# Performance work log

Measured on AMD Instinct MI355X. Metric: run time of the kernel, lower is better.

Reference implementation:

```python
import jax, jax.numpy as jnp
import numpy as np

H, W = 101, 31
HEADS, DH, FREQ = 8, 64, 64
C_DIM = 256
INNER = HEADS * DH
EPS = 1e-5


def _conv2d(x, w, b):
    # x: (B, Cin, H, W), w: (Cout, Cin, 3, 3) -> SAME padding, stride 1
    y = jax.lax.conv_general_dilated(x, w, (1, 1), 'SAME',
                                     dimension_numbers=('NCHW', 'OIHW', 'NCHW'))
    return y + b[None, :, None, None]


def setup_inputs() -> dict:
    key = jax.random.key(0)
    ks = jax.random.split(key, 8)
    B = 32
    N = H * W  # 3131
    s = 0.02
    x = jax.random.normal(ks[0], (B, N, C_DIM), jnp.float32)
    conv_fx_w = jax.random.normal(ks[1], (INNER, C_DIM, 3, 3), jnp.float32) * s
    conv_fx_b = jnp.zeros((INNER,), jnp.float32)
    conv_x_w = jax.random.normal(ks[2], (INNER, C_DIM, 3, 3), jnp.float32) * s
    conv_x_b = jnp.zeros((INNER,), jnp.float32)
    gate_w = jax.random.normal(ks[3], (FREQ, DH), jnp.float32) * s  # nn.Linear weight (out,in)
    gate_b = jnp.zeros((FREQ,), jnp.float32)
    temperature = jnp.full((1, HEADS, 1, 1), 0.5, jnp.float32)
    ln_gamma = jnp.ones((FREQ, DH), jnp.float32)
    ln_beta = jnp.zeros((FREQ, DH), jnp.float32)
    mlp_w = jax.random.normal(ks[4], (DH, DH), jnp.float32) * s
    out_w = jax.random.normal(ks[5], (C_DIM, INNER), jnp.float32) * s
    out_b = jnp.zeros((C_DIM,), jnp.float32)
    # fixed (non-trainable) spectral basis, L2-normalized per row like F.normalize(dim=-1)
    inver = jax.random.normal(ks[6], (N, FREQ), jnp.float32)
    inver = inver / jnp.linalg.norm(inver, axis=-1, keepdims=True)
    return dict(x=x, conv_fx_w=conv_fx_w, conv_fx_b=conv_fx_b, conv_x_w=conv_x_w,
                conv_x_b=conv_x_b, gate_w=gate_w, gate_b=gate_b,
                temperature=temperature, ln_gamma=ln_gamma, ln_beta=ln_beta,
                mlp_w=mlp_w, out_w=out_w, out_b=out_b, inver=inver)


def reference(x, conv_fx_w, conv_fx_b, conv_x_w, conv_x_b, gate_w, gate_b,
              temperature, ln_gamma, ln_beta, mlp_w, out_w, out_b, inver):
    B, N, C = x.shape
    xi = x.reshape(B, H, W, C).transpose(0, 3, 1, 2)  # (B, C, H, W)

    def proj(w, b):
        y = _conv2d(xi, w, b)                                  # (B, inner, H, W)
        return y.transpose(0, 2, 3, 1).reshape(B, N, HEADS, DH).transpose(0, 2, 1, 3)  # (B,h,N,d)

    fx_mid = proj(conv_fx_w, conv_fx_b)
    x_mid = proj(conv_x_w, conv_x_b)

    temp = jnp.clip(temperature, 0.1, 5.0)                      # (1,h,1,1)
    logits = jnp.einsum('bhnc,gc->bhng', x_mid, gate_w) + gate_b
    gate = jax.nn.softmax(logits / temp, axis=-1)               # (B,h,N,g)
    eigens = gate * inver[None, None]                           # (B,h,N,g)

    spec = jnp.einsum('bhnc,bhng->bhgc', fx_mid, eigens)        # (B,h,g,c)
    # LayerNorm over the trailing (g, c) axes jointly
    mu = spec.mean(axis=(-2, -1), keepdims=True)
    var = spec.var(axis=(-2, -1), keepdims=True)
    spec = (spec - mu) * jax.lax.rsqrt(var + EPS) * ln_gamma + ln_beta

    out_spec = jnp.einsum('bhgi,io->bhgo', spec, mlp_w)
    out_x = jnp.einsum('bhgc,bhng->bhnc', out_spec, eigens)     # (B,h,N,c)
    out_x = out_x.transpose(0, 2, 1, 3).reshape(B, N, HEADS * DH)
    return jnp.einsum('bnd,cd->bnc', out_x, out_w) + out_b      # to_out (dropout is identity)
```

## Files before the change

### kernel.cpp

```cpp
#include <hip/hip_runtime.h>
#include <hip/hip_bf16.h>
#include <stdint.h>

#define HH 101
#define WW 31
#define NN 3131
#define NPAD 3136
#define BB 32
#define NH 8
#define CDIM 256
#define GG 64
#define HP 103
#define WP 33

typedef __attribute__((ext_vector_type(8))) short bf16x8;
typedef __attribute__((ext_vector_type(4))) float f32x4;
typedef __attribute__((ext_vector_type(4))) unsigned short ushort4_t;
typedef __attribute__((ext_vector_type(8))) unsigned short ushort8_t;
typedef __attribute__((ext_vector_type(4))) float float4_t;

static __device__ __forceinline__ unsigned short f2bf(float f) {
  union { float f; uint32_t u; } v; v.f = f;
  uint32_t u = v.u;
  return (unsigned short)((u + 0x7fffu + ((u >> 16) & 1u)) >> 16);
}
static __device__ __forceinline__ float bf2f(unsigned short h) {
  union { uint32_t u; float f; } v; v.u = ((uint32_t)h) << 16;
  return v.f;
}
static __device__ __forceinline__ void gload_lds16(const void* g, void* l) {
  __builtin_amdgcn_global_load_lds((const __attribute__((address_space(1))) void*)g,
                                   (__attribute__((address_space(3))) void*)l, 16, 0, 0);
}
static __device__ __forceinline__ int xcd_swz(int bid, int nwg) {
  int q = nwg >> 3, r = nwg & 7;
  int xcd = bid & 7, pos = bid >> 3;
  int base = (xcd < r) ? xcd * (q + 1) : r * (q + 1) + (xcd - r) * q;
  return base + pos;
}

__global__ void k_pad(const float* __restrict__ x, unsigned short* __restrict__ xpad, int b0) {
  const int xx = blockIdx.x, yy = blockIdx.y, b = blockIdx.z;
  const int t = threadIdx.x;
  ushort4_t o; o.x = 0; o.y = 0; o.z = 0; o.w = 0;
  if (yy >= 1 && yy <= HH && xx >= 1 && xx <= WW) {
    const int n = (yy - 1) * WW + (xx - 1);
    const float4_t v = *(const float4_t*)(x + (((int64_t)(b0 + b) * NN + n) * CDIM + t * 4));
    o.x = f2bf(v.x); o.y = f2bf(v.y); o.z = f2bf(v.z); o.w = f2bf(v.w);
  }
  *(ushort4_t*)(xpad + (((int64_t)b * HP + yy) * WP + xx) * CDIM + t * 4) = o;
}

__global__ void k_wpack(const float* __restrict__ fxw, const float* __restrict__ xw,
                        const float* __restrict__ fxb, const float* __restrict__ xb,
                        const float* __restrict__ gw,
                        unsigned short* __restrict__ Wb, float* __restrict__ bias,
                        unsigned short* __restrict__ gwb) {
  int tid = blockIdx.x * blockDim.x + threadIdx.x;
  const int total = 9 * 1024 * 256;
  if (tid < total) {
    int cin = tid & 255; int rest = tid >> 8; int co = rest & 1023; int t = rest >> 10;
    float v = (co < 512) ? fxw[(int64_t)co * 2304 + cin * 9 + t]
                         : xw[(int64_t)(co - 512) * 2304 + cin * 9 + t];
    Wb[tid] = f2bf(v);
  }
  if (tid < 1024) bias[tid] = (tid < 512) ? fxb[tid] : xb[tid - 512];
  if (tid < 4096) gwb[tid] = f2bf(gw[tid]);
}

__global__ void k_pprep(const float* __restrict__ mlp, const float* __restrict__ outw,
                        unsigned short* __restrict__ Pt) {
  int h = blockIdx.x >> 6, i = blockIdx.x & 63, co = threadIdx.x;
  float a = 0.f;
  for (int c = 0; c < 64; ++c) a += mlp[i * 64 + c] * outw[(int64_t)co * 512 + h * 64 + c];
  Pt[((int64_t)h * 256 + co) * 64 + i] = f2bf(a);
}

__global__ void k_padzero(unsigned short* __restrict__ fxT, unsigned short* __restrict__ xmid,
                          int CB) {
  int tid = blockIdx.x * blockDim.x + threadIdx.x;
  if (tid >= CB * 2560) return;
  {
    int j = tid % 5; int rc = tid / 5;
    fxT[(int64_t)rc * NPAD + NN + j] = 0;
  }
  {
    int d = tid & 63; int rest = tid >> 6;
    int j = rest % 5; int bh = rest / 5;
    xmid[((int64_t)bh * NPAD + NN + j) * 64 + d] = 0;
  }
}

__launch_bounds__(512, 2)
__global__ void k_conv8(const unsigned short* __restrict__ xpad,
                        const unsigned short* __restrict__ Wb,
                        const float* __restrict__ bias,
                        unsigned short* __restrict__ fxT,
                        unsigned short* __restrict__ xmid) {
  extern __shared__ unsigned short lds[];
  const int swz = xcd_swz(blockIdx.x, gridDim.x);
  const int r   = swz % 52;
  const int b   = swz / 52;
  const int bx  = r & 3;
  const int mt  = r >> 2;
  const int tid = threadIdx.x, wid = tid >> 6, lane = tid & 63;
  const int wm = wid & 3, wn = wid >> 2;
  const int arow = lane & 15, col16 = lane >> 4;
  const int n00 = mt * 256, co00 = bx * 256;

  const int srow = wid * 16 + (lane >> 2);
  const int tc   = ((lane & 3) ^ ((lane >> 3) & 3)) * 8;
  int na0 = n00 + srow;        if (na0 >= NN) na0 = NN - 1;
  int na1 = n00 + srow + 128;  if (na1 >= NN) na1 = NN - 1;
  const int y0 = na0 / WW, x0v = na0 % WW;
  const int y1 = na1 / WW, x1v = na1 % WW;
  const unsigned short* aS0 = xpad + ((int64_t)(b * HP + y0) * WP + x0v) * CDIM + tc;
  const unsigned short* aS1 = xpad + ((int64_t)(b * HP + y1) * WP + x1v) * CDIM + tc;
  const unsigned short* bS0 = Wb + (int64_t)(co00 + srow) * CDIM + tc;
  const unsigned short* bS1 = Wb + (int64_t)(co00 + srow + 128) * CDIM + tc;

  const int rdsz = (col16 ^ ((arow >> 1) & 3)) * 8;

  f32x4 acc[4][8] = {};
  bf16x8 a0[4], a1[4], b03[4], b47[4];

#define STAGE_A(s, kk, aoffv)                                        \
  { unsigned short* d = lds + (s) * 32768 + (kk) * 8192 + wid * 512; \
    gload_lds16(aS0 + (aoffv) + (kk) * 32, d);                       \
    gload_lds16(aS1 + (aoffv) + (kk) * 32, d + 4096); }
#define STAGE_B(s, kk, boffv)                                                \
  { unsigned short* d = lds + (s) * 32768 + 16384 + (kk) * 8192 + wid * 512; \
    gload_lds16(bS0 + (boffv) + (kk) * 32, d);                               \
    gload_lds16(bS1 + (boffv) + (kk) * 32, d + 4096); }
#define KOFF(ks, aoffv, boffv)                              \
  { const int tap = (ks) >> 2;                              \
    const int dy = (tap >= 6) + (tap >= 3);                 \
    const int dx = tap - dy * 3;                            \
    const int cb = ((ks) & 3) << 6;                         \
    aoffv = (dy * WP + dx) * CDIM + cb;                     \
    boffv = tap * 262144 + cb; }
#define RD_A(dst, s, kk, mf)                                                             \
  dst = *(const bf16x8*)(lds + (s) * 32768 + (kk) * 8192 +                               \
                         (wm * 64 + (mf) * 16 + arow) * 32 + rdsz);
#define RD_B(dst, s, kk, nf)                                                             \
  dst = *(const bf16x8*)(lds + (s) * 32768 + 16384 + (kk) * 8192 +                       \
                         (wn * 128 + (nf) * 16 + arow) * 32 + rdsz);
#define MFMA16(aset, bset, nbase)                                                        \
  __builtin_amdgcn_s_setprio(1);                                                         \
  _Pragma("unroll")                                                                      \
  for (int mf = 0; mf < 4; ++mf) {                                                       \
    _Pragma("unroll")                                                                    \
    for (int nf = 0; nf < 4; ++nf)                                                       \
      acc[mf][(nbase) + nf] =                                                            \
        __builtin_amdgcn_mfma_f32_16x16x32_bf16(aset[mf], bset[nf], acc[mf][(nbase) + nf], 0, 0, 0); \
  }                                                                                      \
  __builtin_amdgcn_s_setprio(0);

  int aoff0, boff0;
  KOFF(0, aoff0, boff0);
  STAGE_A(0, 0, aoff0); STAGE_B(0, 0, boff0);
  STAGE_A(0, 1, aoff0); STAGE_B(0, 1, boff0);
  asm volatile("s_waitcnt vmcnt(4)" ::: "memory");
  __builtin_amdgcn_s_barrier();
  asm volatile("" ::: "memory");
  #pragma unroll
  for (int i = 0; i < 4; ++i) { RD_A(a0[i], 0, 0, i); }
  #pragma unroll
  for (int i = 0; i < 4; ++i) { RD_B(b03[i], 0, 0, i); }

  #pragma unroll 1
  for (int t = 0; t < 36; ++t) {
    const int cur = t & 1, nxt = cur ^ 1;
    const int tn = (t < 35) ? t + 1 : 35;
    int aoffn, boffn;
    KOFF(tn, aoffn, boffn);

    #pragma unroll
    for (int i = 0; i < 4; ++i) { RD_B(b47[i], cur, 0, 4 + i); }
    STAGE_A(nxt, 0, aoffn);
    asm volatile("s_waitcnt lgkmcnt(4)" ::: "memory");
    __builtin_amdgcn_sched_barrier(0);
    MFMA16(a0, b03, 0);

    STAGE_B(nxt, 0, boffn);
    asm volatile("s_waitcnt vmcnt(4)" ::: "memory");
    __builtin_amdgcn_s_barrier();
    asm volatile("" ::: "memory");
    #pragma unroll
    for (int i = 0; i < 4; ++i) { RD_A(a1[i], cur, 1, i); }
    #pragma unroll
    for (int i = 0; i < 4; ++i) { RD_B(b03[i], cur, 1, i); }
    asm volatile("s_waitcnt lgkmcnt(8)" ::: "memory");
    __builtin_amdgcn_sched_barrier(0);
    MFMA16(a0, b47, 4);

    #pragma unroll
    for (int i = 0; i < 4; ++i) { RD_B(b47[i], cur, 1, 4 + i); }
    STAGE_A(nxt, 1, aoffn);
    asm volatile("s_waitcnt lgkmcnt(4)" ::: "memory");
    __builtin_amdgcn_sched_barrier(0);
    MFMA16(a1, b03, 0);

    STAGE_B(nxt, 1, boffn);
    asm volatile("s_waitcnt vmcnt(4)" ::: "memory");
    __builtin_amdgcn_s_barrier();
    asm volatile("" ::: "memory");
    #pragma unroll
    for (int i = 0; i < 4; ++i) { RD_A(a0[i], nxt, 0, i); }
    #pragma unroll
    for (int i = 0; i < 4; ++i) { RD_B(b03[i], nxt, 0, i); }
    asm volatile("s_waitcnt lgkmcnt(8)" ::: "memory");
    __builtin_amdgcn_sched_barrier(0);
    MFMA16(a1, b47, 4);
  }

  asm volatile("s_waitcnt vmcnt(0) lgkmcnt(0)" ::: "memory");

  const int rowoff = col16 * 4;
  #pragma unroll
  for (int mf = 0; mf < 4; ++mf) {
    const int nr = n00 + wm * 64 + mf * 16 + rowoff;
    #pragma unroll
    for (int nf = 0; nf < 8; ++nf) {
      const int co = co00 + wn * 128 + nf * 16 + arow;
      const float bvs = bias[co];
      const float v0 = acc[mf][nf][0] + bvs;
      const float v1 = acc[mf][nf][1] + bvs;
      const float v2 = acc[mf][nf][2] + bvs;
      const float v3 = acc[mf][nf][3] + bvs;
      if (bx < 2) {
        const int h = co >> 6, c = co & 63;
        unsigned short* dst = fxT + ((int64_t)((b * NH + h) * 64 + c)) * NPAD + nr;
        if (nr + 3 < NN) {
          ushort4_t o; o.x = f2bf(v0); o.y = f2bf(v1); o.z = f2bf(v2); o.w = f2bf(v3);
          *(ushort4_t*)dst = o;
        } else {
          if (nr + 0 < NN) dst[0] = f2bf(v0);
          if (nr + 1 < NN) dst[1] = f2bf(v1);
          if (nr + 2 < NN) dst[2] = f2bf(v2);
          if (nr + 3 < NN) dst[3] = f2bf(v3);
        }
      } else {
        const int h = (co >> 6) & 7, d = co & 63;
        unsigned short* dst = xmid + ((int64_t)(b * NH + h) * NPAD + nr) * 64 + d;
        if (nr + 0 < NN) dst[0] = f2bf(v0);
        if (nr + 1 < NN) dst[64] = f2bf(v1);
        if (nr + 2 < NN) dst[128] = f2bf(v2);
        if (nr + 3 < NN) dst[192] = f2bf(v3);
      }
    }
  }
#undef STAGE_A
#undef STAGE_B
#undef KOFF
#undef RD_A
#undef RD_B
#undef MFMA16
}

__global__ void k_eig(const unsigned short* __restrict__ xmid,
                      const unsigned short* __restrict__ gwb,
                      const float* __restrict__ gateb,
                      const float* __restrict__ temperature,
                      const float* __restrict__ inver,
                      unsigned short* __restrict__ eigT,
                      unsigned short* __restrict__ eigN) {
  __shared__ unsigned short egN[64 * 72];
  __shared__ unsigned short egT[64 * 72];
  const int nt = blockIdx.x, h = blockIdx.y, b = blockIdx.z;
  const int tid = threadIdx.x;
  const int w = tid >> 6, lane = tid & 63;
  const int n0 = nt * 64 + w * 16;
  const int bh = b * NH + h;
  float tv = temperature[h];
  tv = fminf(fmaxf(tv, 0.1f), 5.0f);
  const float itemp = 1.0f / tv;
  const int arow = lane & 15;
  const int koff = (lane >> 4) * 8;
  const unsigned short* aptr = xmid + ((int64_t)bh * NPAD + (n0 + arow)) * 64 + koff;
  bf16x8 a0 = *(const bf16x8*)(aptr);
  bf16x8 a1 = *(const bf16x8*)(aptr + 32);
  f32x4 acc[4] = {};
  #pragma unroll
  for (int ng = 0; ng < 4; ++ng) {
    const unsigned short* bptr = gwb + (ng * 16 + arow) * 64 + koff;
    bf16x8 b0 = *(const bf16x8*)(bptr);
    bf16x8 b1 = *(const bf16x8*)(bptr + 32);
    acc[ng] = __builtin_amdgcn_mfma_f32_16x16x32_bf16(a0, b0, acc[ng], 0, 0, 0);
    acc[ng] = __builtin_amdgcn_mfma_f32_16x16x32_bf16(a1, b1, acc[ng], 0, 0, 0);
  }
  #pragma unroll
  for (int r = 0; r < 4; ++r) {
    const int nl = w * 16 + ((lane >> 4) << 2) + r;
    const int n = nt * 64 + nl;
    float vals[4];
    #pragma unroll
    for (int ng = 0; ng < 4; ++ng) vals[ng] = (acc[ng][r] + gateb[ng * 16 + arow]) * itemp;
    float mx = fmaxf(fmaxf(vals[0], vals[1]), fmaxf(vals[2], vals[3]));
    #pragma unroll
    for (int s = 1; s < 16; s <<= 1) mx = fmaxf(mx, __shfl_xor(mx, s));
    float ex[4]; float sum = 0.f;
    #pragma unroll
    for (int ng = 0; ng < 4; ++ng) { ex[ng] = __expf(vals[ng] - mx); sum += ex[ng]; }
    #pragma unroll
    for (int s = 1; s < 16; s <<= 1) sum += __shfl_xor(sum, s);
    const float inv = 1.0f / sum;
    const bool valid = (n < NN);
    #pragma unroll
    for (int ng = 0; ng < 4; ++ng) {
      const int g = ng * 16 + arow;
      float iv = valid ? inver[(int64_t)n * GG + g] : 0.f;
      unsigned short u = valid ? f2bf(ex[ng] * inv * iv) : (unsigned short)0;
      egN[nl * 72 + g] = u;
      egT[g * 72 + nl] = u;
    }
  }
  __syncthreads();
  const int row = tid >> 2, c0 = (tid & 3) << 4;
  {
    ushort8_t v0 = *(ushort8_t*)&egN[row * 72 + c0];
    ushort8_t v1 = *(ushort8_t*)&egN[row * 72 + c0 + 8];
    unsigned short* dst = eigN + ((int64_t)bh * NPAD + nt * 64 + row) * 64 + c0;
    *(ushort8_t*)dst = v0; *(ushort8_t*)(dst + 8) = v1;
  }
  {
    ushort8_t v0 = *(ushort8_t*)&egT[row * 72 + c0];
    ushort8_t v1 = *(ushort8_t*)&egT[row * 72 + c0 + 8];
    unsigned short* dst = eigT + ((int64_t)(bh * 64 + row)) * NPAD + nt * 64 + c0;
    *(ushort8_t*)dst = v0; *(ushort8_t*)(dst + 8) = v1;
  }
}

__launch_bounds__(256, 1)
__global__ void k_specln(const unsigned short* __restrict__ eigT,
                         const unsigned short* __restrict__ fxT,
                         const float* __restrict__ gamma, const float* __restrict__ beta,
                         const unsigned short* __restrict__ Pt,
                         unsigned short* __restrict__ m2t) {
  extern __shared__ char sm[];
  float* sacc = (float*)sm;
  unsigned short* specb = (unsigned short*)(sm + 66560);
  float* red = (float*)(sm + 74752);
  unsigned short* mstrip = (unsigned short*)(sm + 74784);
  const int bhl = blockIdx.x;
  const int h = bhl & 7, bl = bhl >> 3;
  const int tid = threadIdx.x, w = tid >> 6, lane = tid & 63;
  const int arow = lane & 15, col16 = lane >> 4;
  const int koff = col16 * 8;
  const unsigned short* eb = eigT + (int64_t)bhl * 64 * NPAD;
  const unsigned short* fb = fxT + (int64_t)bhl * 64 * NPAD;

  const int ks0 = (98 * w) >> 2, ks1 = (98 * (w + 1)) >> 2;
  f32x4 acc[4][4] = {};
  for (int ks = ks0; ks < ks1; ++ks) {
    const int k0 = ks * 32 + koff;
    bf16x8 av[4], bv[4];
    #pragma unroll
    for (int mg = 0; mg < 4; ++mg) av[mg] = *(const bf16x8*)(eb + (int64_t)(mg * 16 + arow) * NPAD + k0);
    #pragma unroll
    for (int ng = 0; ng < 4; ++ng) bv[ng] = *(const bf16x8*)(fb + (int64_t)(ng * 16 + arow) * NPAD + k0);
    #pragma unroll
    for (int mg = 0; mg < 4; ++mg)
      #pragma unroll
      for (int ng = 0; ng < 4; ++ng)
        acc[mg][ng] = __builtin_amdgcn_mfma_f32_16x16x32_bf16(av[mg], bv[ng], acc[mg][ng], 0, 0, 0);
  }
  float* pw = sacc + w * (64 * 65);
  #pragma unroll
  for (int mg = 0; mg < 4; ++mg)
    #pragma unroll
    for (int ng = 0; ng < 4; ++ng)
      #pragma unroll
      for (int r = 0; r < 4; ++r)
        pw[(mg * 16 + col16 * 4 + r) * 65 + ng * 16 + arow] = acc[mg][ng][r];
  __syncthreads();

  float vloc[16];
  float lsum = 0.f, lsq = 0.f;
  #pragma unroll
  for (int idx = 0; idx < 16; ++idx) {
    const int e = tid + idx * 256;
    const int g = e >> 6, c = e & 63;
    float v = sacc[g * 65 + c] + sacc[4160 + g * 65 + c] +
              sacc[8320 + g * 65 + c] + sacc[12480 + g * 65 + c];
    vloc[idx] = v; lsum += v; lsq += v * v;
  }
  #pragma unroll
  for (int s = 1; s < 64; s <<= 1) { lsum += __shfl_xor(lsum, s); lsq += __shfl_xor(lsq, s); }
  if (lane == 0) { red[w] = lsum; red[4 + w] = lsq; }
  __syncthreads();
  const float tsum = red[0] + red[1] + red[2] + red[3];
  const float tsq = red[4] + red[5] + red[6] + red[7];
  const float mu = tsum * (1.0f / 4096.0f);
  const float var = tsq * (1.0f / 4096.0f) - mu * mu;
  const float rs = rsqrtf(var + 1e-5f);
  #pragma unroll
  for (int idx = 0; idx < 16; ++idx) {
    const int e = tid + idx * 256;
    const int g = e >> 6, c = e & 63;
    float sv = (vloc[idx] - mu) * rs * gamma[e] + beta[e];
    specb[g * 64 + ((((c >> 3) ^ (g & 7))) << 3) + (c & 7)] = f2bf(sv);
  }
  __syncthreads();

  f32x4 a2[4][4] = {};
  const unsigned short* pth = Pt + ((int64_t)h * 256 + w * 64) * 64;
  #pragma unroll
  for (int kk = 0; kk < 2; ++kk) {
    const int i0 = kk * 32 + koff;
    const int i8 = (i0 >> 3);
    bf16x8 av2[4], bv2[4];
    #pragma unroll
    for (int mg = 0; mg < 4; ++mg) {
      const int g = mg * 16 + arow;
      av2[mg] = *(const bf16x8*)(specb + g * 64 + ((i8 ^ (g & 7)) << 3));
    }
    #pragma unroll
    for (int ng = 0; ng < 4; ++ng)
      bv2[ng] = *(const bf16x8*)(pth + (ng * 16 + arow) * 64 + i0);
    #pragma unroll
    for (int mg = 0; mg < 4; ++mg)
      #pragma unroll
      for (int ng = 0; ng < 4; ++ng)
        a2[mg][ng] = __builtin_amdgcn_mfma_f32_16x16x32_bf16(av2[mg], bv2[ng], a2[mg][ng], 0, 0, 0);
  }
  unsigned short* ms = mstrip + w * (64 * 72);
  #pragma unroll
  for (int mg = 0; mg < 4; ++mg)
    #pragma unroll
    for (int ng = 0; ng < 4; ++ng)
      #pragma unroll
      for (int r = 0; r < 4; ++r)
        ms[(ng * 16 + arow) * 72 + mg * 16 + col16 * 4 + r] = f2bf(a2[mg][ng][r]);
  __syncthreads();
  #pragma unroll
  for (int e0 = 0; e0 < 8; ++e0) {
    const int e = lane + e0 * 64;
    const int row = e >> 3, g8 = e & 7;
    ushort8_t v = *(ushort8_t*)&ms[row * 72 + g8 * 8];
    *(ushort8_t*)(m2t + ((int64_t)(bl * 256 + w * 64 + row)) * 512 + h * 64 + g8 * 8) = v;
  }
}

__launch_bounds__(256)
__global__ void k_out(const unsigned short* __restrict__ eigN,
                      const unsigned short* __restrict__ m2t,
                      const float* __restrict__ outb,
                      float* __restrict__ out, int b0) {
  const int swz = xcd_swz(blockIdx.x, gridDim.x);
  const int ct = swz & 1;
  const int mt = (swz >> 1) % 25;
  const int b  = swz / 50;
  const int w = threadIdx.x >> 6, lane = threadIdx.x & 63;
  const int wm = w >> 1, wn = w & 1;
  const int arow = lane & 15, koff = (lane >> 4) * 8;
  const int co0 = ct * 128 + wn * 64;
  const int n0 = mt * 128 + wm * 64;
  f32x4 acc[4][4] = {};
  const unsigned short* ebase = eigN + (int64_t)b * NH * NPAD * 64;
  const unsigned short* mbase = m2t + (int64_t)b * 256 * 512;
  for (int ks = 0; ks < 16; ++ks) {
    const int hh = ks >> 1;
    const int g0 = (ks & 1) * 32 + koff;
    bf16x8 av[4], bv[4];
    #pragma unroll
    for (int mg = 0; mg < 4; ++mg) {
      int n = n0 + mg * 16 + arow;
      if (n > NPAD - 1) n = NPAD - 1;
      av[mg] = *(const bf16x8*)(ebase + ((int64_t)hh * NPAD + n) * 64 + g0);
    }
    #pragma unroll
    for (int ng = 0; ng < 4; ++ng)
      bv[ng] = *(const bf16x8*)(mbase + (int64_t)(co0 + ng * 16 + arow) * 512 + ks * 32 + koff);
    #pragma unroll
    for (int mg = 0; mg < 4; ++mg)
      #pragma unroll
      for (int ng = 0; ng < 4; ++ng)
        acc[mg][ng] = __builtin_amdgcn_mfma_f32_16x16x32_bf16(av[mg], bv[ng], acc[mg][ng], 0, 0, 0);
  }
  #pragma unroll
  for (int mg = 0; mg < 4; ++mg) {
    const int nr = n0 + mg * 16 + ((lane >> 4) << 2);
    #pragma unroll
    for (int ng = 0; ng < 4; ++ng) {
      const int co = co0 + ng * 16 + arow;
      const float bv = outb[co];
      #pragma unroll
      for (int r = 0; r < 4; ++r) {
        if (nr + r < NN)
          out[((int64_t)(b0 + b) * NN + nr + r) * 256 + co] = acc[mg][ng][r] + bv;
      }
    }
  }
}

extern "C" void kernel_launch(void* const* d_in, const int* in_sizes, int n_in,
                              void* d_out, int out_size, void* d_ws, size_t ws_size,
                              hipStream_t stream) {
  const float* x     = (const float*)d_in[0];
  const float* fxw   = (const float*)d_in[1];
  const float* fxb   = (const float*)d_in[2];
  const float* xw    = (const float*)d_in[3];
  const float* xb    = (const float*)d_in[4];
  const float* gw    = (const float*)d_in[5];
  const float* gb    = (const float*)d_in[6];
  const float* temp  = (const float*)d_in[7];
  const float* gamma = (const float*)d_in[8];
  const float* beta  = (const float*)d_in[9];
  const float* mlp   = (const float*)d_in[10];
  const float* outw  = (const float*)d_in[11];
  const float* outb  = (const float*)d_in[12];
  const float* inver = (const float*)d_in[13];
  float* out = (float*)d_out;
  char* ws = (char*)d_ws;
  (void)in_sizes; (void)n_in; (void)out_size;

  hipFuncSetAttribute(reinterpret_cast<const void*>(k_conv8),
                      hipFuncAttributeMaxDynamicSharedMemorySize, 131072);
  hipFuncSetAttribute(reinterpret_cast<const void*>(k_specln),
                      hipFuncAttributeMaxDynamicSharedMemorySize, 131072);

  int CB = 1;
  {
    const int cands[6] = {32, 16, 8, 4, 2, 1};
    for (int i = 0; i < 6; ++i) {
      unsigned long long need = 4993024ull + (unsigned long long)cands[i] * 14847488ull;
      if (need <= (unsigned long long)ws_size) { CB = cands[i]; break; }
    }
  }

  unsigned short* Wb   = (unsigned short*)(ws + 0);
  float*          bias = (float*)(ws + 4718592);
  unsigned short* gwb  = (unsigned short*)(ws + 4722688);
  unsigned short* Pt   = (unsigned short*)(ws + 4730880);
  const size_t F0      = 4993024;
  const size_t szXpad  = (size_t)CB * 1740288;
  const size_t szM2t   = (size_t)CB * 262144;
  const size_t szBig   = (size_t)CB * 3211264;
  unsigned short* xpad = (unsigned short*)(ws + F0);
  unsigned short* m2t  = (unsigned short*)(ws + F0 + szXpad);
  unsigned short* fxT  = (unsigned short*)(ws + F0 + szXpad + szM2t);
  unsigned short* xmid = (unsigned short*)(ws + F0 + szXpad + szM2t + szBig);
  unsigned short* eigT = (unsigned short*)(ws + F0 + szXpad + szM2t + 2 * szBig);
  unsigned short* eigN = (unsigned short*)(ws + F0 + szXpad + szM2t + 3 * szBig);

  k_wpack<<<dim3(9216), dim3(256), 0, stream>>>(fxw, xw, fxb, xb, gw, Wb, bias, gwb);
  k_pprep<<<dim3(512), dim3(256), 0, stream>>>(mlp, outw, Pt);

  for (int b0 = 0; b0 < BB; b0 += CB) {
    k_pad<<<dim3(WP, HP, CB), dim3(64), 0, stream>>>(x, xpad, b0);
    k_padzero<<<dim3(CB * 10), dim3(256), 0, stream>>>(fxT, xmid, CB);
    k_conv8<<<dim3(52 * CB), dim3(512), 131072, stream>>>(xpad, Wb, bias, fxT, xmid);
    k_eig<<<dim3(49, 8, CB), dim3(256), 0, stream>>>(xmid, gwb, gb, temp, inver, eigT, eigN);
    k_specln<<<dim3(CB * 8), dim3(256), 111648, stream>>>(eigT, fxT, gamma, beta, Pt, m2t);
    k_out<<<dim3(50 * CB), dim3(256), 0, stream>>>(eigN, m2t, outb, out, b0);
  }
}
```

Baseline: 884.9 us.

## Enlarge per-wave conv tile to 128x128 using four waves per block

The implicit-GEMM convolution kernel moves from 8 waves (512 threads) to 4 waves (256 threads) per 256x256 block tile. Each wave now computes a 128x128 sub-tile with 64 accumulators instead of 32, and loads four rows per staging step. The aim is to cut LDS reads per MFMA and raise arithmetic intensity per wave. In exchange, accumulator registers per thread double and fewer waves are available per CU to hide latency, with launch bounds set to one block.

```diff
diff --git a/kernel.cpp b/kernel.cpp
--- a/kernel.cpp
+++ b/kernel.cpp
@@ -91,7 +91,7 @@
   }
 }
 
-__launch_bounds__(512, 2)
+__launch_bounds__(256, 1)
 __global__ void k_conv8(const unsigned short* __restrict__ xpad,
                         const unsigned short* __restrict__ Wb,
                         const float* __restrict__ bias,
@@ -104,34 +104,39 @@
   const int bx  = r & 3;
   const int mt  = r >> 2;
   const int tid = threadIdx.x, wid = tid >> 6, lane = tid & 63;
-  const int wm = wid & 3, wn = wid >> 2;
+  const int wm = wid >> 1, wn = wid & 1;
   const int arow = lane & 15, col16 = lane >> 4;
   const int n00 = mt * 256, co00 = bx * 256;
 
-  const int srow = wid * 16 + (lane >> 2);
-  const int tc   = ((lane & 3) ^ ((lane >> 3) & 3)) * 8;
-  int na0 = n00 + srow;        if (na0 >= NN) na0 = NN - 1;
-  int na1 = n00 + srow + 128;  if (na1 >= NN) na1 = NN - 1;
-  const int y0 = na0 / WW, x0v = na0 % WW;
-  const int y1 = na1 / WW, x1v = na1 % WW;
-  const unsigned short* aS0 = xpad + ((int64_t)(b * HP + y0) * WP + x0v) * CDIM + tc;
-  const unsigned short* aS1 = xpad + ((int64_t)(b * HP + y1) * WP + x1v) * CDIM + tc;
-  const unsigned short* bS0 = Wb + (int64_t)(co00 + srow) * CDIM + tc;
-  const unsigned short* bS1 = Wb + (int64_t)(co00 + srow + 128) * CDIM + tc;
+  const int tc = ((lane & 3) ^ ((lane >> 3) & 3)) * 8;
+  const unsigned short* aS[4];
+  const unsigned short* bS[4];
+  #pragma unroll
+  for (int i = 0; i < 4; ++i) {
+    const int srow = wid * 64 + i * 16 + (lane >> 2);
+    int na = n00 + srow; if (na >= NN) na = NN - 1;
+    const int y = na / WW, xv = na % WW;
+    aS[i] = xpad + ((int64_t)(b * HP + y) * WP + xv) * CDIM + tc;
+    bS[i] = Wb + (int64_t)(co00 + srow) * CDIM + tc;
+  }
 
   const int rdsz = (col16 ^ ((arow >> 1) & 3)) * 8;
 
-  f32x4 acc[4][8] = {};
-  bf16x8 a0[4], a1[4], b03[4], b47[4];
-
-#define STAGE_A(s, kk, aoffv)                                        \
-  { unsigned short* d = lds + (s) * 32768 + (kk) * 8192 + wid * 512; \
-    gload_lds16(aS0 + (aoffv) + (kk) * 32, d);                       \
-    gload_lds16(aS1 + (aoffv) + (kk) * 32, d + 4096); }
-#define STAGE_B(s, kk, boffv)                                                \
-  { unsigned short* d = lds + (s) * 32768 + 16384 + (kk) * 8192 + wid * 512; \
-    gload_lds16(bS0 + (boffv) + (kk) * 32, d);                               \
-    gload_lds16(bS1 + (boffv) + (kk) * 32, d + 4096); }
+  f32x4 acc[8][8] = {};
+  bf16x8 a0[8], a1[8], b03[4], b47[4];
+
+#define STAGE_A(s, kk, aoffv)                                          \
+  { unsigned short* d = lds + (s) * 32768 + (kk) * 8192 + wid * 2048;  \
+    gload_lds16(aS[0] + (aoffv) + (kk) * 32, d);                       \
+    gload_lds16(aS[1] + (aoffv) + (kk) * 32, d + 512);                 \
+    gload_lds16(aS[2] + (aoffv) + (kk) * 32, d + 1024);                \
+    gload_lds16(aS[3] + (aoffv) + (kk) * 32, d + 1536); }
+#define STAGE_B(s, kk, boffv)                                                  \
+  { unsigned short* d = lds + (s) * 32768 + 16384 + (kk) * 8192 + wid * 2048;  \
+    gload_lds16(bS[0] + (boffv) + (kk) * 32, d);                               \
+    gload_lds16(bS[1] + (boffv) + (kk) * 32, d + 512);                         \
+    gload_lds16(bS[2] + (boffv) + (kk) * 32, d + 1024);                        \
+    gload_lds16(bS[3] + (boffv) + (kk) * 32, d + 1536); }
 #define KOFF(ks, aoffv, boffv)                              \
   { const int tap = (ks) >> 2;                              \
     const int dy = (tap >= 6) + (tap >= 3);                 \
@@ -139,32 +144,32 @@
     const int cb = ((ks) & 3) << 6;                         \
     aoffv = (dy * WP + dx) * CDIM + cb;                     \
     boffv = tap * 262144 + cb; }
-#define RD_A(dst, s, kk, mf)                                                             \
-  dst = *(const bf16x8*)(lds + (s) * 32768 + (kk) * 8192 +                               \
-                         (wm * 64 + (mf) * 16 + arow) * 32 + rdsz);
-#define RD_B(dst, s, kk, nf)                                                             \
-  dst = *(const bf16x8*)(lds + (s) * 32768 + 16384 + (kk) * 8192 +                       \
+#define RD_A(dst, s, kk, mf)                                                       \
+  dst = *(const bf16x8*)(lds + (s) * 32768 + (kk) * 8192 +                         \
+                         (wm * 128 + (mf) * 16 + arow) * 32 + rdsz);
+#define RD_B(dst, s, kk, nf)                                                       \
+  dst = *(const bf16x8*)(lds + (s) * 32768 + 16384 + (kk) * 8192 +                 \
                          (wn * 128 + (nf) * 16 + arow) * 32 + rdsz);
-#define MFMA16(aset, bset, nbase)                                                        \
-  __builtin_amdgcn_s_setprio(1);                                                         \
-  _Pragma("unroll")                                                                      \
-  for (int mf = 0; mf < 4; ++mf) {                                                       \
-    _Pragma("unroll")                                                                    \
-    for (int nf = 0; nf < 4; ++nf)                                                       \
-      acc[mf][(nbase) + nf] =                                                            \
-        __builtin_amdgcn_mfma_f32_16x16x32_bf16(aset[mf], bset[nf], acc[mf][(nbase) + nf], 0, 0, 0); \
-  }                                                                                      \
+#define MFMA32(aset, bset, nbase)                                                  \
+  __builtin_amdgcn_s_setprio(1);                                                   \
+  _Pragma("unroll")                                                                \
+  for (int mf = 0; mf < 8; ++mf) {                                                 \
+    _Pragma("unroll")                                                              \
+    for (int j = 0; j < 4; ++j)                                                    \
+      acc[mf][(nbase) + j] =                                                       \
+        __builtin_amdgcn_mfma_f32_16x16x32_bf16(aset[mf], bset[j], acc[mf][(nbase) + j], 0, 0, 0); \
+  }                                                                                \
   __builtin_amdgcn_s_setprio(0);
 
   int aoff0, boff0;
   KOFF(0, aoff0, boff0);
   STAGE_A(0, 0, aoff0); STAGE_B(0, 0, boff0);
   STAGE_A(0, 1, aoff0); STAGE_B(0, 1, boff0);
-  asm volatile("s_waitcnt vmcnt(4)" ::: "memory");
+  asm volatile("s_waitcnt vmcnt(8)" ::: "memory");
   __builtin_amdgcn_s_barrier();
   asm volatile("" ::: "memory");
   #pragma unroll
-  for (int i = 0; i < 4; ++i) { RD_A(a0[i], 0, 0, i); }
+  for (int i = 0; i < 8; ++i) { RD_A(a0[i], 0, 0, i); }
   #pragma unroll
   for (int i = 0; i < 4; ++i) { RD_B(b03[i], 0, 0, i); }
 
@@ -180,46 +185,46 @@
     STAGE_A(nxt, 0, aoffn);
     asm volatile("s_waitcnt lgkmcnt(4)" ::: "memory");
     __builtin_amdgcn_sched_barrier(0);
-    MFMA16(a0, b03, 0);
+    MFMA32(a0, b03, 0);
 
     STAGE_B(nxt, 0, boffn);
-    asm volatile("s_waitcnt vmcnt(4)" ::: "memory");
+    asm volatile("s_waitcnt vmcnt(8)" ::: "memory");
     __builtin_amdgcn_s_barrier();
     asm volatile("" ::: "memory");
     #pragma unroll
-    for (int i = 0; i < 4; ++i) { RD_A(a1[i], cur, 1, i); }
+    for (int i = 0; i < 8; ++i) { RD_A(a1[i], cur, 1, i); }
     #pragma unroll
     for (int i = 0; i < 4; ++i) { RD_B(b03[i], cur, 1, i); }
-    asm volatile("s_waitcnt lgkmcnt(8)" ::: "memory");
+    asm volatile("s_waitcnt lgkmcnt(12)" ::: "memory");
     __builtin_amdgcn_sched_barrier(0);
-    MFMA16(a0, b47, 4);
+    MFMA32(a0, b47, 4);
 
     #pragma unroll
     for (int i = 0; i < 4; ++i) { RD_B(b47[i], cur, 1, 4 + i); }
     STAGE_A(nxt, 1, aoffn);
     asm volatile("s_waitcnt lgkmcnt(4)" ::: "memory");
     __builtin_amdgcn_sched_barrier(0);
-    MFMA16(a1, b03, 0);
+    MFMA32(a1, b03, 0);
 
     STAGE_B(nxt, 1, boffn);
-    asm volatile("s_waitcnt vmcnt(4)" ::: "memory");
+    asm volatile("s_waitcnt vmcnt(8)" ::: "memory");
     __builtin_amdgcn_s_barrier();
     asm volatile("" ::: "memory");
     #pragma unroll
-    for (int i = 0; i < 4; ++i) { RD_A(a0[i], nxt, 0, i); }
+    for (int i = 0; i < 8; ++i) { RD_A(a0[i], nxt, 0, i); }
     #pragma unroll
     for (int i = 0; i < 4; ++i) { RD_B(b03[i], nxt, 0, i); }
-    asm volatile("s_waitcnt lgkmcnt(8)" ::: "memory");
+    asm volatile("s_waitcnt lgkmcnt(12)" ::: "memory");
     __builtin_amdgcn_sched_barrier(0);
-    MFMA16(a1, b47, 4);
+    MFMA32(a1, b47, 4);
   }
 
   asm volatile("s_waitcnt vmcnt(0) lgkmcnt(0)" ::: "memory");
 
   const int rowoff = col16 * 4;
   #pragma unroll
-  for (int mf = 0; mf < 4; ++mf) {
-    const int nr = n00 + wm * 64 + mf * 16 + rowoff;
+  for (int mf = 0; mf < 8; ++mf) {
+    const int nr = n00 + wm * 128 + mf * 16 + rowoff;
     #pragma unroll
     for (int nf = 0; nf < 8; ++nf) {
       const int co = co00 + wn * 128 + nf * 16 + arow;
@@ -255,7 +260,7 @@
 #undef KOFF
 #undef RD_A
 #undef RD_B
-#undef MFMA16
+#undef MFMA32
 }
 
 __global__ void k_eig(const unsigned short* __restrict__ xmid,
@@ -550,7 +555,7 @@
   for (int b0 = 0; b0 < BB; b0 += CB) {
     k_pad<<<dim3(WP, HP, CB), dim3(64), 0, stream>>>(x, xpad, b0);
     k_padzero<<<dim3(CB * 10), dim3(256), 0, stream>>>(fxT, xmid, CB);
-    k_conv8<<<dim3(52 * CB), dim3(512), 131072, stream>>>(xpad, Wb, bias, fxT, xmid);
+    k_conv8<<<dim3(52 * CB), dim3(256), 131072, stream>>>(xpad, Wb, bias, fxT, xmid);
     k_eig<<<dim3(49, 8, CB), dim3(256), 0, stream>>>(xmid, gwb, gb, temp, inver, eigT, eigN);
     k_specln<<<dim3(CB * 8), dim3(256), 111648, stream>>>(eigT, fxT, gamma, beta, Pt, m2t);
     k_out<<<dim3(50 * CB), dim3(256), 0, stream>>>(eigN, m2t, outb, out, b0);
```

New measurement: 968.3 us. 1.09x slower.

## Load conv weight fragments directly from global into registers, stage only activations in LDS

Applied to the files above, without the earlier changes.

The conv GEMM kernel stops staging the weight (B) tiles through LDS and has each wave load its B fragments straight from global memory into registers. LDS now holds only the double-buffered activation tiles, which halves dynamic shared memory from 128 KB to 64 KB and removes the B-side LDS reads. The intent is to cut LDS traffic and footprint, possibly allowing more occupancy. The cost is global/L2 latency on the B loads, which each wave issues redundantly, plus larger register pressure from four B fragment sets and a simpler interleave that waits lgkmcnt(0).

```diff
diff --git a/kernel.cpp b/kernel.cpp
--- a/kernel.cpp
+++ b/kernel.cpp
@@ -116,22 +116,17 @@
   const int y1 = na1 / WW, x1v = na1 % WW;
   const unsigned short* aS0 = xpad + ((int64_t)(b * HP + y0) * WP + x0v) * CDIM + tc;
   const unsigned short* aS1 = xpad + ((int64_t)(b * HP + y1) * WP + x1v) * CDIM + tc;
-  const unsigned short* bS0 = Wb + (int64_t)(co00 + srow) * CDIM + tc;
-  const unsigned short* bS1 = Wb + (int64_t)(co00 + srow + 128) * CDIM + tc;
+  const unsigned short* baseB = Wb + (int64_t)(co00 + wn * 128 + arow) * 256 + col16 * 8;
 
   const int rdsz = (col16 ^ ((arow >> 1) & 3)) * 8;
 
   f32x4 acc[4][8] = {};
-  bf16x8 a0[4], a1[4], b03[4], b47[4];
+  bf16x8 a0[4], a1[4], bq0[4], bq1[4], bq2[4], bq3[4];
 
 #define STAGE_A(s, kk, aoffv)                                        \
-  { unsigned short* d = lds + (s) * 32768 + (kk) * 8192 + wid * 512; \
+  { unsigned short* d = lds + (s) * 16384 + (kk) * 8192 + wid * 512; \
     gload_lds16(aS0 + (aoffv) + (kk) * 32, d);                       \
     gload_lds16(aS1 + (aoffv) + (kk) * 32, d + 4096); }
-#define STAGE_B(s, kk, boffv)                                                \
-  { unsigned short* d = lds + (s) * 32768 + 16384 + (kk) * 8192 + wid * 512; \
-    gload_lds16(bS0 + (boffv) + (kk) * 32, d);                               \
-    gload_lds16(bS1 + (boffv) + (kk) * 32, d + 4096); }
 #define KOFF(ks, aoffv, boffv)                              \
   { const int tap = (ks) >> 2;                              \
     const int dy = (tap >= 6) + (tap >= 3);                 \
@@ -139,34 +134,34 @@
     const int cb = ((ks) & 3) << 6;                         \
     aoffv = (dy * WP + dx) * CDIM + cb;                     \
     boffv = tap * 262144 + cb; }
-#define RD_A(dst, s, kk, mf)                                                             \
-  dst = *(const bf16x8*)(lds + (s) * 32768 + (kk) * 8192 +                               \
-                         (wm * 64 + (mf) * 16 + arow) * 32 + rdsz);
-#define RD_B(dst, s, kk, nf)                                                             \
-  dst = *(const bf16x8*)(lds + (s) * 32768 + 16384 + (kk) * 8192 +                       \
-                         (wn * 128 + (nf) * 16 + arow) * 32 + rdsz);
-#define MFMA16(aset, bset, nbase)                                                        \
-  __builtin_amdgcn_s_setprio(1);                                                         \
-  _Pragma("unroll")                                                                      \
-  for (int mf = 0; mf < 4; ++mf) {                                                       \
-    _Pragma("unroll")                                                                    \
-    for (int nf = 0; nf < 4; ++nf)                                                       \
-      acc[mf][(nbase) + nf] =                                                            \
+#define LDB(dst, boffv, kk, nf4)                                                    \
+  { _Pragma("unroll")                                                               \
+    for (int j = 0; j < 4; ++j)                                                     \
+      dst[j] = *(const bf16x8*)(baseB + ((nf4) + j) * 4096 + (boffv) + (kk) * 32); }
+#define RD_A4(dst, s, kk)                                                           \
+  { _Pragma("unroll")                                                               \
+    for (int i = 0; i < 4; ++i)                                                     \
+      dst[i] = *(const bf16x8*)(lds + (s) * 16384 + (kk) * 8192 +                   \
+                                (wm * 64 + i * 16 + arow) * 32 + rdsz); }
+#define MFMA16(aset, bset, nbase)                                                   \
+  __builtin_amdgcn_s_setprio(1);                                                    \
+  _Pragma("unroll")                                                                 \
+  for (int mf = 0; mf < 4; ++mf) {                                                  \
+    _Pragma("unroll")                                                               \
+    for (int nf = 0; nf < 4; ++nf)                                                  \
+      acc[mf][(nbase) + nf] =                                                       \
         __builtin_amdgcn_mfma_f32_16x16x32_bf16(aset[mf], bset[nf], acc[mf][(nbase) + nf], 0, 0, 0); \
-  }                                                                                      \
+  }                                                                                 \
   __builtin_amdgcn_s_setprio(0);
 
-  int aoff0, boff0;
-  KOFF(0, aoff0, boff0);
-  STAGE_A(0, 0, aoff0); STAGE_B(0, 0, boff0);
-  STAGE_A(0, 1, aoff0); STAGE_B(0, 1, boff0);
+  int aoff0, boffc;
+  KOFF(0, aoff0, boffc);
+  STAGE_A(0, 0, aoff0);
+  STAGE_A(0, 1, aoff0);
+  LDB(bq0, boffc, 0, 0);
   asm volatile("s_waitcnt vmcnt(4)" ::: "memory");
   __builtin_amdgcn_s_barrier();
   asm volatile("" ::: "memory");
-  #pragma unroll
-  for (int i = 0; i < 4; ++i) { RD_A(a0[i], 0, 0, i); }
-  #pragma unroll
-  for (int i = 0; i < 4; ++i) { RD_B(b03[i], 0, 0, i); }
 
   #pragma unroll 1
   for (int t = 0; t < 36; ++t) {
@@ -175,43 +170,29 @@
     int aoffn, boffn;
     KOFF(tn, aoffn, boffn);
 
-    #pragma unroll
-    for (int i = 0; i < 4; ++i) { RD_B(b47[i], cur, 0, 4 + i); }
+    LDB(bq1, boffc, 0, 4);
     STAGE_A(nxt, 0, aoffn);
-    asm volatile("s_waitcnt lgkmcnt(4)" ::: "memory");
+    STAGE_A(nxt, 1, aoffn);
+    RD_A4(a0, cur, 0);
+    asm volatile("s_waitcnt lgkmcnt(0)" ::: "memory");
     __builtin_amdgcn_sched_barrier(0);
-    MFMA16(a0, b03, 0);
-
-    STAGE_B(nxt, 0, boffn);
+    MFMA16(a0, bq0, 0);
+
+    LDB(bq2, boffc, 1, 0);
+    RD_A4(a1, cur, 1);
+    MFMA16(a0, bq1, 4);
+
+    LDB(bq3, boffc, 1, 4);
+    asm volatile("s_waitcnt lgkmcnt(0)" ::: "memory");
+    __builtin_amdgcn_sched_barrier(0);
+    MFMA16(a1, bq2, 0);
+
+    LDB(bq0, boffn, 0, 0);
+    MFMA16(a1, bq3, 4);
     asm volatile("s_waitcnt vmcnt(4)" ::: "memory");
     __builtin_amdgcn_s_barrier();
     asm volatile("" ::: "memory");
-    #pragma unroll
-    for (int i = 0; i < 4; ++i) { RD_A(a1[i], cur, 1, i); }
-    #pragma unroll
-    for (int i = 0; i < 4; ++i) { RD_B(b03[i], cur, 1, i); }
-    asm volatile("s_waitcnt lgkmcnt(8)" ::: "memory");
-    __builtin_amdgcn_sched_barrier(0);
-    MFMA16(a0, b47, 4);
-
-    #pragma unroll
-    for (int i = 0; i < 4; ++i) { RD_B(b47[i], cur, 1, 4 + i); }
-    STAGE_A(nxt, 1, aoffn);
-    asm volatile("s_waitcnt lgkmcnt(4)" ::: "memory");
-    __builtin_amdgcn_sched_barrier(0);
-    MFMA16(a1, b03, 0);
-
-    STAGE_B(nxt, 1, boffn);
-    asm volatile("s_waitcnt vmcnt(4)" ::: "memory");
-    __builtin_amdgcn_s_barrier();
-    asm volatile("" ::: "memory");
-    #pragma unroll
-    for (int i = 0; i < 4; ++i) { RD_A(a0[i], nxt, 0, i); }
-    #pragma unroll
-    for (int i = 0; i < 4; ++i) { RD_B(b03[i], nxt, 0, i); }
-    asm volatile("s_waitcnt lgkmcnt(8)" ::: "memory");
-    __builtin_amdgcn_sched_barrier(0);
-    MFMA16(a1, b47, 4);
+    boffc = boffn;
   }
 
   asm volatile("s_waitcnt vmcnt(0) lgkmcnt(0)" ::: "memory");
@@ -251,10 +232,9 @@
     }
   }
 #undef STAGE_A
-#undef STAGE_B
 #undef KOFF
-#undef RD_A
-#undef RD_B
+#undef LDB
+#undef RD_A4
 #undef MFMA16
 }
 
@@ -516,7 +496,7 @@
   (void)in_sizes; (void)n_in; (void)out_size;
 
   hipFuncSetAttribute(reinterpret_cast<const void*>(k_conv8),
-                      hipFuncAttributeMaxDynamicSharedMemorySize, 131072);
+                      hipFuncAttributeMaxDynamicSharedMemorySize, 65536);
   hipFuncSetAttribute(reinterpret_cast<const void*>(k_specln),
                       hipFuncAttributeMaxDynamicSharedMemorySize, 131072);
 
@@ -550,7 +530,7 @@
   for (int b0 = 0; b0 < BB; b0 += CB) {
     k_pad<<<dim3(WP, HP, CB), dim3(64), 0, stream>>>(x, xpad, b0);
     k_padzero<<<dim3(CB * 10), dim3(256), 0, stream>>>(fxT, xmid, CB);
-    k_conv8<<<dim3(52 * CB), dim3(512), 131072, stream>>>(xpad, Wb, bias, fxT, xmid);
+    k_conv8<<<dim3(52 * CB), dim3(512), 65536, stream>>>(xpad, Wb, bias, fxT, xmid);
     k_eig<<<dim3(49, 8, CB), dim3(256), 0, stream>>>(xmid, gwb, gb, temp, inver, eigT, eigN);
     k_specln<<<dim3(CB * 8), dim3(256), 111648, stream>>>(eigT, fxT, gamma, beta, Pt, m2t);
     k_out<<<dim3(50 * CB), dim3(256), 0, stream>>>(eigN, m2t, outb, out, b0);
```

After: 1.509 ms. 70.5% more time.

## Fuse gate softmax and eigen computation into conv epilogue, dropping xmid buffer

Applied to the files above, without the earlier changes.

The x-projection half of the conv kernel no longer writes x_mid to global memory. It stages each head's tile in LDS, runs the gate matmul with MFMA, applies the temperature softmax times the basis, and writes eigT and eigN directly. This removes the separate k_eig launch and the round trip of the x_mid tensor through global memory, and it shrinks the workspace so larger batch chunks can fit. In exchange the x-projection blocks get a heavier epilogue with extra barriers and register pressure, which makes their work uneven against the fx blocks.

```diff
diff --git a/kernel.cpp b/kernel.cpp
--- a/kernel.cpp
+++ b/kernel.cpp
@@ -76,27 +76,24 @@
   Pt[((int64_t)h * 256 + co) * 64 + i] = f2bf(a);
 }
 
-__global__ void k_padzero(unsigned short* __restrict__ fxT, unsigned short* __restrict__ xmid,
-                          int CB) {
+__global__ void k_padzero(unsigned short* __restrict__ fxT, int CB) {
   int tid = blockIdx.x * blockDim.x + threadIdx.x;
   if (tid >= CB * 2560) return;
-  {
-    int j = tid % 5; int rc = tid / 5;
-    fxT[(int64_t)rc * NPAD + NN + j] = 0;
-  }
-  {
-    int d = tid & 63; int rest = tid >> 6;
-    int j = rest % 5; int bh = rest / 5;
-    xmid[((int64_t)bh * NPAD + NN + j) * 64 + d] = 0;
-  }
+  int j = tid % 5; int rc = tid / 5;
+  fxT[(int64_t)rc * NPAD + NN + j] = 0;
 }
 
 __launch_bounds__(512, 2)
 __global__ void k_conv8(const unsigned short* __restrict__ xpad,
                         const unsigned short* __restrict__ Wb,
                         const float* __restrict__ bias,
+                        const unsigned short* __restrict__ gwb,
+                        const float* __restrict__ gateb,
+                        const float* __restrict__ temperature,
+                        const float* __restrict__ inver,
                         unsigned short* __restrict__ fxT,
-                        unsigned short* __restrict__ xmid) {
+                        unsigned short* __restrict__ eigT,
+                        unsigned short* __restrict__ eigN) {
   extern __shared__ unsigned short lds[];
   const int swz = xcd_swz(blockIdx.x, gridDim.x);
   const int r   = swz % 52;
@@ -217,18 +214,19 @@
   asm volatile("s_waitcnt vmcnt(0) lgkmcnt(0)" ::: "memory");
 
   const int rowoff = col16 * 4;
-  #pragma unroll
-  for (int mf = 0; mf < 4; ++mf) {
-    const int nr = n00 + wm * 64 + mf * 16 + rowoff;
-    #pragma unroll
-    for (int nf = 0; nf < 8; ++nf) {
-      const int co = co00 + wn * 128 + nf * 16 + arow;
-      const float bvs = bias[co];
-      const float v0 = acc[mf][nf][0] + bvs;
-      const float v1 = acc[mf][nf][1] + bvs;
-      const float v2 = acc[mf][nf][2] + bvs;
-      const float v3 = acc[mf][nf][3] + bvs;
-      if (bx < 2) {
+
+  if (bx < 2) {
+    #pragma unroll
+    for (int mf = 0; mf < 4; ++mf) {
+      const int nr = n00 + wm * 64 + mf * 16 + rowoff;
+      #pragma unroll
+      for (int nf = 0; nf < 8; ++nf) {
+        const int co = co00 + wn * 128 + nf * 16 + arow;
+        const float bvs = bias[co];
+        const float v0 = acc[mf][nf][0] + bvs;
+        const float v1 = acc[mf][nf][1] + bvs;
+        const float v2 = acc[mf][nf][2] + bvs;
+        const float v3 = acc[mf][nf][3] + bvs;
         const int h = co >> 6, c = co & 63;
         unsigned short* dst = fxT + ((int64_t)((b * NH + h) * 64 + c)) * NPAD + nr;
         if (nr + 3 < NN) {
@@ -240,13 +238,103 @@
           if (nr + 2 < NN) dst[2] = f2bf(v2);
           if (nr + 3 < NN) dst[3] = f2bf(v3);
         }
-      } else {
-        const int h = (co >> 6) & 7, d = co & 63;
-        unsigned short* dst = xmid + ((int64_t)(b * NH + h) * NPAD + nr) * 64 + d;
-        if (nr + 0 < NN) dst[0] = f2bf(v0);
-        if (nr + 1 < NN) dst[64] = f2bf(v1);
-        if (nr + 2 < NN) dst[128] = f2bf(v2);
-        if (nr + 3 < NN) dst[192] = f2bf(v3);
+      }
+    }
+  } else {
+    const int hbase = (bx - 2) * 4;
+    unsigned short* xm = lds;
+    #pragma unroll 1
+    for (int hh = 0; hh < 2; ++hh) {
+      __syncthreads();
+      unsigned short* xmw = xm + wn * (256 * 72);
+      #pragma unroll
+      for (int mf = 0; mf < 4; ++mf) {
+        const int nr = wm * 64 + mf * 16 + rowoff;
+        #pragma unroll
+        for (int j = 0; j < 4; ++j) {
+          const int nf = hh * 4 + j;
+          const int co = co00 + wn * 128 + nf * 16 + arow;
+          const float bvs = bias[co];
+          const int d = j * 16 + arow;
+          #pragma unroll
+          for (int r2 = 0; r2 < 4; ++r2)
+            xmw[(nr + r2) * 72 + d] = f2bf(acc[mf][nf][r2] + bvs);
+        }
+      }
+      __syncthreads();
+      const int hg = hbase + wn * 2 + hh;
+      float tv = temperature[hg];
+      tv = fminf(fmaxf(tv, 0.1f), 5.0f);
+      const float itemp = 1.0f / tv;
+      f32x4 acc2[4][4] = {};
+      #pragma unroll
+      for (int kk = 0; kk < 2; ++kk) {
+        bf16x8 av2[4], bv2[4];
+        #pragma unroll
+        for (int mg = 0; mg < 4; ++mg)
+          av2[mg] = *(const bf16x8*)(xmw + (wm * 64 + mg * 16 + arow) * 72 + kk * 32 + col16 * 8);
+        #pragma unroll
+        for (int ng = 0; ng < 4; ++ng)
+          bv2[ng] = *(const bf16x8*)(gwb + (ng * 16 + arow) * 64 + kk * 32 + col16 * 8);
+        #pragma unroll
+        for (int mg = 0; mg < 4; ++mg)
+          #pragma unroll
+          for (int ng = 0; ng < 4; ++ng)
+            acc2[mg][ng] = __builtin_amdgcn_mfma_f32_16x16x32_bf16(av2[mg], bv2[ng], acc2[mg][ng], 0, 0, 0);
+      }
+      #pragma unroll
+      for (int mg = 0; mg < 4; ++mg) {
+        unsigned short evq[4][4];
+        #pragma unroll
+        for (int r2 = 0; r2 < 4; ++r2) {
+          const int nl = wm * 64 + mg * 16 + rowoff + r2;
+          const int n = n00 + nl;
+          float vals[4];
+          #pragma unroll
+          for (int ng = 0; ng < 4; ++ng)
+            vals[ng] = (acc2[mg][ng][r2] + gateb[ng * 16 + arow]) * itemp;
+          float mx = fmaxf(fmaxf(vals[0], vals[1]), fmaxf(vals[2], vals[3]));
+          #pragma unroll
+          for (int s = 1; s < 16; s <<= 1) mx = fmaxf(mx, __shfl_xor(mx, s));
+          float ex[4]; float sum = 0.f;
+          #pragma unroll
+          for (int ng = 0; ng < 4; ++ng) { ex[ng] = __expf(vals[ng] - mx); sum += ex[ng]; }
+          #pragma unroll
+          for (int s = 1; s < 16; s <<= 1) sum += __shfl_xor(sum, s);
+          const float inv = 1.0f / sum;
+          const bool valid = (n < NN);
+          #pragma unroll
+          for (int ng = 0; ng < 4; ++ng) {
+            const int g = ng * 16 + arow;
+            float iv = valid ? inver[(int64_t)n * GG + g] : 0.f;
+            unsigned short u = valid ? f2bf(ex[ng] * inv * iv) : (unsigned short)0;
+            evq[ng][r2] = u;
+            xmw[nl * 72 + g] = u;
+          }
+        }
+        const int n0q = n00 + wm * 64 + mg * 16 + rowoff;
+        if (n0q < NPAD) {
+          #pragma unroll
+          for (int ng = 0; ng < 4; ++ng) {
+            const int g = ng * 16 + arow;
+            ushort4_t o; o.x = evq[ng][0]; o.y = evq[ng][1]; o.z = evq[ng][2]; o.w = evq[ng][3];
+            *(ushort4_t*)(eigT + ((int64_t)((b * NH + hg) * 64 + g)) * NPAD + n0q) = o;
+          }
+        }
+      }
+      __syncthreads();
+      {
+        const int wn2 = tid >> 8;
+        const int rr = tid & 255;
+        const int n = n00 + rr;
+        if (n < NPAD) {
+          const int hg2 = hbase + wn2 * 2 + hh;
+          const unsigned short* src = xm + wn2 * (256 * 72) + rr * 72;
+          unsigned short* dst = eigN + ((int64_t)((b * NH + hg2)) * NPAD + n) * 64;
+          #pragma unroll
+          for (int c0 = 0; c0 < 64; c0 += 8)
+            *(ushort8_t*)(dst + c0) = *(const ushort8_t*)(src + c0);
+        }
       }
     }
   }
@@ -256,79 +344,6 @@
 #undef RD_A
 #undef RD_B
 #undef MFMA16
-}
-
-__global__ void k_eig(const unsigned short* __restrict__ xmid,
-                      const unsigned short* __restrict__ gwb,
-                      const float* __restrict__ gateb,
-                      const float* __restrict__ temperature,
-                      const float* __restrict__ inver,
-                      unsigned short* __restrict__ eigT,
-                      unsigned short* __restrict__ eigN) {
-  __shared__ unsigned short egN[64 * 72];
-  __shared__ unsigned short egT[64 * 72];
-  const int nt = blockIdx.x, h = blockIdx.y, b = blockIdx.z;
-  const int tid = threadIdx.x;
-  const int w = tid >> 6, lane = tid & 63;
-  const int n0 = nt * 64 + w * 16;
-  const int bh = b * NH + h;
-  float tv = temperature[h];
-  tv = fminf(fmaxf(tv, 0.1f), 5.0f);
-  const float itemp = 1.0f / tv;
-  const int arow = lane & 15;
-  const int koff = (lane >> 4) * 8;
-  const unsigned short* aptr = xmid + ((int64_t)bh * NPAD + (n0 + arow)) * 64 + koff;
-  bf16x8 a0 = *(const bf16x8*)(aptr);
-  bf16x8 a1 = *(const bf16x8*)(aptr + 32);
-  f32x4 acc[4] = {};
-  #pragma unroll
-  for (int ng = 0; ng < 4; ++ng) {
-    const unsigned short* bptr = gwb + (ng * 16 + arow) * 64 + koff;
-    bf16x8 b0 = *(const bf16x8*)(bptr);
-    bf16x8 b1 = *(const bf16x8*)(bptr + 32);
-    acc[ng] = __builtin_amdgcn_mfma_f32_16x16x32_bf16(a0, b0, acc[ng], 0, 0, 0);
-    acc[ng] = __builtin_amdgcn_mfma_f32_16x16x32_bf16(a1, b1, acc[ng], 0, 0, 0);
-  }
-  #pragma unroll
-  for (int r = 0; r < 4; ++r) {
-    const int nl = w * 16 + ((lane >> 4) << 2) + r;
-    const int n = nt * 64 + nl;
-    float vals[4];
-    #pragma unroll
-    for (int ng = 0; ng < 4; ++ng) vals[ng] = (acc[ng][r] + gateb[ng * 16 + arow]) * itemp;
-    float mx = fmaxf(fmaxf(vals[0], vals[1]), fmaxf(vals[2], vals[3]));
-    #pragma unroll
-    for (int s = 1; s < 16; s <<= 1) mx = fmaxf(mx, __shfl_xor(mx, s));
-    float ex[4]; float sum = 0.f;
-    #pragma unroll
-    for (int ng = 0; ng < 4; ++ng) { ex[ng] = __expf(vals[ng] - mx); sum += ex[ng]; }
-    #pragma unroll
-    for (int s = 1; s < 16; s <<= 1) sum += __shfl_xor(sum, s);
-    const float inv = 1.0f / sum;
-    const bool valid = (n < NN);
-    #pragma unroll
-    for (int ng = 0; ng < 4; ++ng) {
-      const int g = ng * 16 + arow;
-      float iv = valid ? inver[(int64_t)n * GG + g] : 0.f;
-      unsigned short u = valid ? f2bf(ex[ng] * inv * iv) : (unsigned short)0;
-      egN[nl * 72 + g] = u;
-      egT[g * 72 + nl] = u;
-    }
-  }
-  __syncthreads();
-  const int row = tid >> 2, c0 = (tid & 3) << 4;
-  {
-    ushort8_t v0 = *(ushort8_t*)&egN[row * 72 + c0];
-    ushort8_t v1 = *(ushort8_t*)&egN[row * 72 + c0 + 8];
-    unsigned short* dst = eigN + ((int64_t)bh * NPAD + nt * 64 + row) * 64 + c0;
-    *(ushort8_t*)dst = v0; *(ushort8_t*)(dst + 8) = v1;
-  }
-  {
-    ushort8_t v0 = *(ushort8_t*)&egT[row * 72 + c0];
-    ushort8_t v1 = *(ushort8_t*)&egT[row * 72 + c0 + 8];
-    unsigned short* dst = eigT + ((int64_t)(bh * 64 + row)) * NPAD + nt * 64 + c0;
-    *(ushort8_t*)dst = v0; *(ushort8_t*)(dst + 8) = v1;
-  }
 }
 
 __launch_bounds__(256, 1)
@@ -524,7 +539,7 @@
   {
     const int cands[6] = {32, 16, 8, 4, 2, 1};
     for (int i = 0; i < 6; ++i) {
-      unsigned long long need = 4993024ull + (unsigned long long)cands[i] * 14847488ull;
+      unsigned long long need = 4993024ull + (unsigned long long)cands[i] * 11636224ull;
       if (need <= (unsigned long long)ws_size) { CB = cands[i]; break; }
     }
   }
@@ -540,18 +555,17 @@
   unsigned short* xpad = (unsigned short*)(ws + F0);
   unsigned short* m2t  = (unsigned short*)(ws + F0 + szXpad);
   unsigned short* fxT  = (unsigned short*)(ws + F0 + szXpad + szM2t);
-  unsigned short* xmid = (unsigned short*)(ws + F0 + szXpad + szM2t + szBig);
-  unsigned short* eigT = (unsigned short*)(ws + F0 + szXpad + szM2t + 2 * szBig);
-  unsigned short* eigN = (unsigned short*)(ws + F0 + szXpad + szM2t + 3 * szBig);
+  unsigned short* eigT = (unsigned short*)(ws + F0 + szXpad + szM2t + szBig);
+  unsigned short* eigN = (unsigned short*)(ws + F0 + szXpad + szM2t + 2 * szBig);
 
   k_wpack<<<dim3(9216), dim3(256), 0, stream>>>(fxw, xw, fxb, xb, gw, Wb, bias, gwb);
   k_pprep<<<dim3(512), dim3(256), 0, stream>>>(mlp, outw, Pt);
 
   for (int b0 = 0; b0 < BB; b0 += CB) {
     k_pad<<<dim3(WP, HP, CB), dim3(64), 0, stream>>>(x, xpad, b0);
-    k_padzero<<<dim3(CB * 10), dim3(256), 0, stream>>>(fxT, xmid, CB);
-    k_conv8<<<dim3(52 * CB), dim3(512), 131072, stream>>>(xpad, Wb, bias, fxT, xmid);
-    k_eig<<<dim3(49, 8, CB), dim3(256), 0, stream>>>(xmid, gwb, gb, temp, inver, eigT, eigN);
+    k_padzero<<<dim3(CB * 10), dim3(256), 0, stream>>>(fxT, CB);
+    k_conv8<<<dim3(52 * CB), dim3(512), 131072, stream>>>(xpad, Wb, bias, gwb, gb, temp,
+                                                          inver, fxT, eigT, eigN);
     k_specln<<<dim3(CB * 8), dim3(256), 111648, stream>>>(eigT, fxT, gamma, beta, Pt, m2t);
     k_out<<<dim3(50 * CB), dim3(256), 0, stream>>>(eigN, m2t, outb, out, b0);
   }
```

New measurement: 1.191 ms. 1.35x slower.
